# Kernel optimization log

Measured on AMD Instinct MI355X. Metric: run time of the kernel, lower is better.

## Reference

```python
import jax, jax.numpy as jnp
import numpy as np

DIM = 2048
NUM_HEADS = 8
HEAD_DIM = DIM // NUM_HEADS  # 256; forward requires seq_len == HEAD_DIM
B = 64
N = HEAD_DIM  # q @ k (untransposed) only works when N == head_dim


def setup_inputs() -> dict:
    key = jax.random.key(0)
    k1, k2, k3, k4 = jax.random.split(key, 4)
    x = jax.random.normal(k1, (B, N, DIM), dtype=jnp.float32)
    # torch Linear stores weight as [out_features, in_features]
    w_qkv = jax.random.normal(k2, (3 * DIM, DIM), dtype=jnp.float32) * 0.02
    w_proj = jax.random.normal(k3, (DIM, DIM), dtype=jnp.float32) * 0.02
    b_proj = jax.random.normal(k4, (DIM,), dtype=jnp.float32) * 0.02
    return {"x": x, "w_qkv": w_qkv, "w_proj": w_proj, "b_proj": b_proj}


def reference(x, w_qkv, w_proj, b_proj):
    Bb, Nn, C = x.shape
    H, D = NUM_HEADS, C // NUM_HEADS
    # qkv projection (no bias), split into q,k,v of shape [B,H,N,D]
    qkv = (x @ w_qkv.T).reshape(Bb, Nn, 3, H, D).transpose(2, 0, 3, 1, 4)
    q, k, v = qkv[0], qkv[1], qkv[2]
    # NON-standard: q @ k with k NOT transposed -> contracts q's feature dim
    # against k's token dim (valid because D == N). attn: [B,H,N,N]
    attn = jnp.matmul(q, k)
    # transpose last two dims, then softmax over the new last axis
    attn = jnp.swapaxes(attn, -2, -1)
    attn = jax.nn.softmax(attn, axis=-1)
    out = jnp.matmul(attn, v)              # [B,H,N,D]
    out = out.swapaxes(1, 2).reshape(Bb, Nn, C)
    return out @ w_proj.T + b_proj
```

## Files before the change

### kernel.cpp

```cpp
#include <hip/hip_runtime.h>
#include <hip/hip_bf16.h>

typedef unsigned short u16;
typedef __attribute__((ext_vector_type(4))) float f32x4;
typedef __attribute__((ext_vector_type(8))) short short8;
typedef __attribute__((ext_vector_type(8))) u16 us8;


__device__ __forceinline__ u16 f2bf(float f) {
  union { float f; unsigned u; } v; v.f = f;
  unsigned r = v.u + 0x7fffu + ((v.u >> 16) & 1u);
  return (u16)(r >> 16);
}
__device__ __forceinline__ float bf2f(u16 h) {
  union { unsigned u; float f; } v; v.u = ((unsigned)h) << 16; return v.f;
}

__global__ void beacon_kernel(float* __restrict__ out, float val, int n) {
  int stride = gridDim.x * blockDim.x;
  for (int i = blockIdx.x * blockDim.x + threadIdx.x; i < n; i += stride)
    out[i] = val;
}

__global__ void split_kernel(const float* __restrict__ in, u16* __restrict__ hi,
                             u16* __restrict__ lo, int n4) {
  int stride = gridDim.x * blockDim.x;
  for (int i = blockIdx.x * blockDim.x + threadIdx.x; i < n4; i += stride) {
    f32x4 v = ((const f32x4*)in)[i];
    ushort4 h;
    h.x = f2bf(v[0]); h.y = f2bf(v[1]); h.z = f2bf(v[2]); h.w = f2bf(v[3]);
    ((ushort4*)hi)[i] = h;
    if (lo) {
      ushort4 l;
      l.x = f2bf(v[0] - bf2f(h.x)); l.y = f2bf(v[1] - bf2f(h.y));
      l.z = f2bf(v[2] - bf2f(h.z)); l.w = f2bf(v[3] - bf2f(h.w));
      ((ushort4*)lo)[i] = l;
    }
  }
}

#define SCHED0 __builtin_amdgcn_sched_barrier(0)
#define LGKM0 do { asm volatile("s_waitcnt lgkmcnt(0)" ::: "memory"); SCHED0; } while (0)
#define VM8 do { asm volatile("s_waitcnt vmcnt(8)" ::: "memory"); } while (0)
#define VM4 do { asm volatile("s_waitcnt vmcnt(4)" ::: "memory"); } while (0)
#define VM0 do { asm volatile("s_waitcnt vmcnt(0)" ::: "memory"); } while (0)
#define BAR __builtin_amdgcn_s_barrier()

template<int EPI>
__global__ __launch_bounds__(512, 2)
void gemm256(const u16* __restrict__ A0, const u16* __restrict__ A1,
             const u16* __restrict__ B0, const u16* __restrict__ B1,
             int ldA, int ldB, int ntiles, int segShift, int gridMx,
             u16* __restrict__ qh, u16* __restrict__ ql,
             u16* __restrict__ kh, u16* __restrict__ kl,
             u16* __restrict__ vv,
             float* __restrict__ fout, const float* __restrict__ bias) {
  extern __shared__ __align__(16) u16 lds[];

  const int tid = threadIdx.x;
  const int w = tid >> 6, lane = tid & 63;
  const int wr = w >> 2, wcn = w & 3;
  const int l15 = lane & 15, g = lane >> 4;
  const int rsl = (g + l15) & 3;
  const int scol = ((((tid & 3) - ((tid >> 2) & 3)) & 3) << 3);

  int bid = blockIdx.x, cpx = gridDim.x >> 3;
  int swz = (bid & 7) * cpx + (bid >> 3);
  int m0 = (swz % gridMx) << 8;
  int n0 = (swz / gridMx) << 8;

  const u16* As[2] = {A0, A1};
  const u16* Bs[2] = {B0, B1};
  const int kmask = (1 << segShift) - 1;

  f32x4 acc[8][4] = {};
  short8 af[8], bfr[4];

  auto stage = [&](int db, const u16* Ab, const u16* Bb, int k0) {
    #pragma unroll
    for (int s = 0; s < 2; ++s) {
      const u16* srcA = Ab + (size_t)(m0 + s * 128 + (tid >> 2)) * ldA + k0 + scol;
      u16* dstA = lds + db * 16384 + s * 4096 + tid * 8;
      __builtin_amdgcn_global_load_lds(
          (const __attribute__((address_space(1))) unsigned*)srcA,
          (__attribute__((address_space(3))) unsigned*)dstA, 16, 0, 0);
      const u16* srcB = Bb + (size_t)(n0 + s * 128 + (tid >> 2)) * ldB + k0 + scol;
      u16* dstB = lds + db * 16384 + 8192 + s * 4096 + tid * 8;
      __builtin_amdgcn_global_load_lds(
          (const __attribute__((address_space(1))) unsigned*)srcB,
          (__attribute__((address_space(3))) unsigned*)dstB, 16, 0, 0);
    }
  };
  auto readAB = [&](int db) {
    const u16* base = lds + db * 16384;
    #pragma unroll
    for (int i = 0; i < 8; ++i) {
      int row = wr * 128 + i * 16 + l15;
      af[i] = *(const short8*)(base + row * 32 + rsl * 8);
    }
    #pragma unroll
    for (int j = 0; j < 4; ++j) {
      int row = wcn * 64 + j * 16 + l15;
      bfr[j] = *(const short8*)(base + 8192 + row * 32 + rsl * 8);
    }
  };

#define MMA_ALL                                                                \
  __builtin_amdgcn_s_setprio(1);                                               \
  _Pragma("unroll") for (int i = 0; i < 8; ++i)                                \
    _Pragma("unroll") for (int j = 0; j < 4; ++j)                              \
      acc[i][j] = __builtin_amdgcn_mfma_f32_16x16x32_bf16(                     \
          af[i], bfr[j], acc[i][j], 0, 0, 0);                                  \
  __builtin_amdgcn_s_setprio(0)

  const int T = ntiles;
  #pragma unroll
  for (int p = 0; p < 3; ++p)
    stage(p, As[p >> segShift], Bs[p >> segShift], (p & kmask) << 5);

  for (int t = 0; t < T - 3; ++t) {
    VM8; BAR; SCHED0;
    readAB(t & 3);
    int t3 = t + 3;
    stage(t3 & 3, As[t3 >> segShift], Bs[t3 >> segShift], (t3 & kmask) << 5);
    LGKM0;
    MMA_ALL;
  }
  VM8; BAR; SCHED0; readAB((T - 3) & 3); LGKM0; MMA_ALL;
  VM4; BAR; SCHED0; readAB((T - 2) & 3); LGKM0; MMA_ALL;
  VM0; BAR; SCHED0; readAB((T - 1) & 3); LGKM0; MMA_ALL;
#undef MMA_ALL

  #pragma unroll
  for (int i = 0; i < 8; ++i)
    #pragma unroll
    for (int j = 0; j < 4; ++j)
      #pragma unroll
      for (int rr = 0; rr < 4; ++rr) {
        int gm = m0 + wr * 128 + i * 16 + g * 4 + rr;
        int gn = n0 + wcn * 64 + j * 16 + l15;
        float val = acc[i][j][rr];
        if constexpr (EPI == 0) {
          int b = gm >> 8, tok = gm & 255;
          int sel = gn >> 11, head = (gn >> 8) & 7, col = gn & 255;
          size_t addr = (((size_t)b * 8 + head) * 256 + tok) * 256 + col;
          u16 h = f2bf(val), lo = f2bf(val - bf2f(h));
          if (sel == 0) { qh[addr] = h; ql[addr] = lo; }
          else          { kh[addr] = h; kl[addr] = lo; }
        } else if constexpr (EPI == 1) {
          int b = gm >> 8, tok = gm & 255;
          int head = (gn >> 8) & 7, col = gn & 255;
          size_t addr = (((size_t)b * 8 + head) * 256 + tok) * 256 + col;
          vv[addr] = f2bf(val);
        } else {
          fout[(size_t)gm * 2048 + gn] = val + bias[gn];
        }
      }
}

template<int EPI, int SWZ>
__global__ __launch_bounds__(256)
void gemm_nt(const u16* __restrict__ A0, const u16* __restrict__ A1, const u16* __restrict__ A2,
             const u16* __restrict__ B0, const u16* __restrict__ B1, const u16* __restrict__ B2,
             float* __restrict__ sout, u16* __restrict__ aout,
             int ksteps, int segShift, int plane_base) {
  __shared__ __align__(16) u16 lds[8192];
  u16* sA = lds;
  u16* sB = lds + 4096;

  const int tid = threadIdx.x;
  const int wave = tid >> 6, lane = tid & 63;
  const int wr = wave >> 1, wc = wave & 1;
  const int l15 = lane & 15, l16 = lane >> 4;
  const int sxor = (l15 >> 1) & 3;

  size_t zoffA = 0, zoffB = 0;
  if constexpr (EPI == 2) {
    size_t gz = (size_t)(plane_base + blockIdx.z) * 65536;
    zoffA = gz; zoffB = gz;
  }
  if constexpr (EPI == 3) {
    zoffA = (size_t)blockIdx.z * 65536;
    zoffB = (size_t)(plane_base + blockIdx.z) * 65536;
  }
  const u16* As[3] = {A0 + zoffA, A1 + zoffA, A2 + zoffA};
  const u16* Bs[3] = {B0 + zoffB, B1 + zoffB, B2 + zoffB};

  const int m0 = blockIdx.x << 7;
  const int n0 = blockIdx.y << 7;
  const int kmask = (1 << segShift) - 1;

  f32x4 acc[4][4] = {};

  auto stage = [&](const u16* gp, int ld, u16* slot, int row0, int k0) {
    int scol = ((lane & 3) ^ ((lane >> 3) & 3)) * 8;
    #pragma unroll
    for (int c = 0; c < 2; ++c) {
      int chunk = wave + c * 4;
      int r = chunk * 16 + (lane >> 2);
      const u16* src = gp + (size_t)(row0 + r) * ld + (k0 + scol);
      __builtin_amdgcn_global_load_lds(
          (const __attribute__((address_space(1))) unsigned*)src,
          (__attribute__((address_space(3))) unsigned*)(slot + chunk * 512), 16, 0, 0);
    }
  };

  for (int ks = 0; ks < ksteps; ++ks) {
    int seg = ks >> segShift;
    int k0 = (ks & kmask) * 32;
    stage(As[seg], 256, sA, m0, k0);
    stage(Bs[seg], 256, sB, n0, k0);
    __syncthreads();

    short8 a[4], b[4];
    #pragma unroll
    for (int i = 0; i < 4; ++i) {
      int ra = (wr * 64 + i * 16 + l15) * 4 + (l16 ^ sxor);
      int rb = (wc * 64 + i * 16 + l15) * 4 + (l16 ^ sxor);
      a[i] = ((const short8*)sA)[ra];
      b[i] = ((const short8*)sB)[rb];
    }
    #pragma unroll
    for (int i = 0; i < 4; ++i)
      #pragma unroll
      for (int j = 0; j < 4; ++j)
        acc[i][j] = __builtin_amdgcn_mfma_f32_16x16x32_bf16(a[i], b[j], acc[i][j], 0, 0, 0);
    __syncthreads();
  }

  #pragma unroll
  for (int i = 0; i < 4; ++i)
    #pragma unroll
    for (int j = 0; j < 4; ++j)
      #pragma unroll
      for (int r = 0; r < 4; ++r) {
        int gm = m0 + wr * 64 + i * 16 + l16 * 4 + r;
        int gn = n0 + wc * 64 + j * 16 + l15;
        float val = acc[i][j][r];
        if constexpr (EPI == 2) {
          sout[(size_t)blockIdx.z * 65536 + (size_t)gm * 256 + gn] = val;
        } else {
          int gp = plane_base + blockIdx.z;
          size_t row = (size_t)(gp >> 3) * 256 + gm;
          size_t col = (size_t)(gp & 7) * 256 + gn;
          aout[row * 2048 + col] = f2bf(val);
        }
      }
}

__global__ void transpose_inplace(u16* __restrict__ kh, u16* __restrict__ kl,
                                  u16* __restrict__ v) {
  __shared__ u16 ta[64][66], tb[64][66];
  u16* base = (blockIdx.z == 0) ? kh : (blockIdx.z == 1) ? kl : v;
  u16* pl = base + (size_t)blockIdx.y * 65536;
  const int RA[10] = {0,1,2,3, 0,0,0,1,1,2};
  const int CA[10] = {0,1,2,3, 1,2,3,2,3,3};
  int p = blockIdx.x;
  int R = RA[p], C = CA[p];
  bool diag = (R == C);
  int tid = threadIdx.x;
  int r = tid >> 2, c0 = (tid & 3) * 16;

  const us8* sa = (const us8*)(pl + (size_t)(R * 64 + r) * 256 + C * 64 + c0);
  us8 a0 = sa[0], a1 = sa[1];
  #pragma unroll
  for (int s = 0; s < 8; ++s) { ta[r][c0 + s] = a0[s]; ta[r][c0 + 8 + s] = a1[s]; }
  if (!diag) {
    const us8* sb = (const us8*)(pl + (size_t)(C * 64 + r) * 256 + R * 64 + c0);
    us8 b0 = sb[0], b1 = sb[1];
    #pragma unroll
    for (int s = 0; s < 8; ++s) { tb[r][c0 + s] = b0[s]; tb[r][c0 + 8 + s] = b1[s]; }
  }
  __syncthreads();
  us8 o0, o1;
  #pragma unroll
  for (int s = 0; s < 8; ++s) { o0[s] = ta[c0 + s][r]; o1[s] = ta[c0 + 8 + s][r]; }
  us8* da = (us8*)(pl + (size_t)(C * 64 + r) * 256 + R * 64 + c0);
  da[0] = o0; da[1] = o1;
  if (!diag) {
    us8 p0, p1;
    #pragma unroll
    for (int s = 0; s < 8; ++s) { p0[s] = tb[c0 + s][r]; p1[s] = tb[c0 + 8 + s][r]; }
    us8* db = (us8*)(pl + (size_t)(R * 64 + r) * 256 + C * 64 + c0);
    db[0] = p0; db[1] = p1;
  }
}

__global__ void softmax_kernel(const float* __restrict__ S, u16* __restrict__ P) {
  int row = blockIdx.x * 4 + (threadIdx.x >> 6);
  int lane = threadIdx.x & 63;
  f32x4 v = ((const f32x4*)(S + (size_t)row * 256))[lane];
  float mx = fmaxf(fmaxf(v[0], v[1]), fmaxf(v[2], v[3]));
  #pragma unroll
  for (int o = 32; o > 0; o >>= 1) mx = fmaxf(mx, __shfl_xor(mx, o));
  float e0 = __expf(v[0] - mx), e1 = __expf(v[1] - mx);
  float e2 = __expf(v[2] - mx), e3 = __expf(v[3] - mx);
  float sum = e0 + e1 + e2 + e3;
  #pragma unroll
  for (int o = 32; o > 0; o >>= 1) sum += __shfl_xor(sum, o);
  float inv = 1.0f / sum;
  ushort4 p;
  p.x = f2bf(e0 * inv); p.y = f2bf(e1 * inv); p.z = f2bf(e2 * inv); p.w = f2bf(e3 * inv);
  ((ushort4*)(P + (size_t)row * 256))[lane] = p;
}

extern "C" void kernel_launch(void* const* d_in, const int* in_sizes, int n_in,
                              void* d_out, int out_size, void* d_ws, size_t ws_size,
                              hipStream_t stream) {
  const float* x  = (const float*)d_in[0];
  const float* wq = (const float*)d_in[1];
  const float* wp = (const float*)d_in[2];
  const float* bp = (const float*)d_in[3];
  float* out = (float*)d_out;
  char* ws = (char*)d_ws;

  const size_t MB = 1ull << 20;
  const size_t NEED = 432 * MB;
  if (ws_size < NEED) {
    beacon_kernel<<<2048, 256, 0, stream>>>(out, (float)(ws_size >> 20), 16384 * 2048);
    return;
  }

  u16* q_hi = (u16*)(ws);
  u16* q_lo = (u16*)(ws + 64 * MB);
  u16* k_hi = (u16*)(ws + 128 * MB);
  u16* k_lo = (u16*)(ws + 192 * MB);
  u16* vbuf = (u16*)(ws + 256 * MB);
  u16* x_hi = (u16*)(ws + 320 * MB);
  u16* w_hi = (u16*)(ws + 384 * MB);
  u16* w_lo = (u16*)(ws + 408 * MB);
  float* S  = (float*)(ws + 320 * MB);
  u16* Pm   = (u16*)(ws + 352 * MB);
  u16* attn = (u16*)(ws + 368 * MB);
  u16* wpb  = (u16*)(ws + 320 * MB);

  split_kernel<<<8192, 256, 0, stream>>>(x,  x_hi, nullptr, 16384 * 2048 / 4);
  split_kernel<<<4096, 256, 0, stream>>>(wq, w_hi, w_lo, 6144 * 2048 / 4);

  gemm256<0><<<1024, 512, 131072, stream>>>(
      x_hi, x_hi, w_hi, w_lo, 2048, 2048, 128, 6, 64,
      q_hi, q_lo, k_hi, k_lo, nullptr, nullptr, nullptr);
  const u16* wv = w_hi + (size_t)4096 * 2048;
  gemm256<1><<<512, 512, 131072, stream>>>(
      x_hi, x_hi, wv, wv, 2048, 2048, 64, 6, 64,
      nullptr, nullptr, nullptr, nullptr, vbuf, nullptr, nullptr);

  transpose_inplace<<<dim3(10, 512, 3), 256, 0, stream>>>(k_hi, k_lo, vbuf);

  for (int gp = 0; gp < 4; ++gp) {
    int pb = gp * 128;
    gemm_nt<2, 0><<<dim3(2, 2, 128), 256, 0, stream>>>(
        k_hi, k_hi, k_lo, q_hi, q_lo, q_hi,
        S, nullptr, 24, 3, pb);
    softmax_kernel<<<8192, 256, 0, stream>>>(S, Pm);
    gemm_nt<3, 0><<<dim3(2, 2, 128), 256, 0, stream>>>(
        Pm, Pm, Pm, vbuf, vbuf, vbuf,
        nullptr, attn, 8, 3, pb);
  }

  split_kernel<<<2048, 256, 0, stream>>>(wp, wpb, nullptr, 2048 * 2048 / 4);
  gemm256<2><<<512, 512, 131072, stream>>>(
      attn, attn, wpb, wpb, 2048, 2048, 64, 6, 64,
      nullptr, nullptr, nullptr, nullptr, nullptr, out, bp);
}
```

Before: 1.179 ms.

## Restructure 256x256 GEMM into K=64 tiles with quadrant-phased 8-wave ping-pong pipeline

Rewrites the main 256x256 bf16 GEMM mainloop to use K=64 tiles split into four 128-row half-buffers (A halves, B halves), double-buffered by tile parity. Each K tile is processed in four quadrant phases where waves read a quarter of the operands, issue the next half-tile load, and run 16 MFMAs. This interleaves global-to-LDS loads with compute at finer granularity and uses an XOR swizzle over 8 slots to avoid bank conflicts. It adds many more barriers per tile, and the per-wave output mapping changes from 128x64 to four 64x32 quadrants, which may add sync overhead.

```diff
diff --git a/kernel.cpp b/kernel.cpp
--- a/kernel.cpp
+++ b/kernel.cpp
@@ -41,15 +41,14 @@
 
 #define SCHED0 __builtin_amdgcn_sched_barrier(0)
 #define LGKM0 do { asm volatile("s_waitcnt lgkmcnt(0)" ::: "memory"); SCHED0; } while (0)
-#define VM8 do { asm volatile("s_waitcnt vmcnt(8)" ::: "memory"); } while (0)
-#define VM4 do { asm volatile("s_waitcnt vmcnt(4)" ::: "memory"); } while (0)
+#define VM6 do { asm volatile("s_waitcnt vmcnt(6)" ::: "memory"); } while (0)
 #define VM0 do { asm volatile("s_waitcnt vmcnt(0)" ::: "memory"); } while (0)
 #define BAR __builtin_amdgcn_s_barrier()
 
 template<int EPI>
 __global__ __launch_bounds__(512, 2)
-void gemm256(const u16* __restrict__ A0, const u16* __restrict__ A1,
-             const u16* __restrict__ B0, const u16* __restrict__ B1,
+void gemm256(const u16* __restrict__ A0p, const u16* __restrict__ A1p,
+             const u16* __restrict__ B0p, const u16* __restrict__ B1p,
              int ldA, int ldB, int ntiles, int segShift, int gridMx,
              u16* __restrict__ qh, u16* __restrict__ ql,
              u16* __restrict__ kh, u16* __restrict__ kl,
@@ -59,77 +58,128 @@
 
   const int tid = threadIdx.x;
   const int w = tid >> 6, lane = tid & 63;
-  const int wr = w >> 2, wcn = w & 3;
+  const int qr = w >> 2, qc = w & 3;
   const int l15 = lane & 15, g = lane >> 4;
-  const int rsl = (g + l15) & 3;
-  const int scol = ((((tid & 3) - ((tid >> 2) & 3)) & 3) << 3);
+  const int rsw = l15 & 7;
+  const int scol = (((tid & 7) ^ ((tid >> 3) & 7)) << 3);
 
   int bid = blockIdx.x, cpx = gridDim.x >> 3;
   int swz = (bid & 7) * cpx + (bid >> 3);
   int m0 = (swz % gridMx) << 8;
   int n0 = (swz / gridMx) << 8;
 
-  const u16* As[2] = {A0, A1};
-  const u16* Bs[2] = {B0, B1};
+  const u16* As[2] = {A0p, A1p};
+  const u16* Bs[2] = {B0p, B1p};
   const int kmask = (1 << segShift) - 1;
 
   f32x4 acc[8][4] = {};
-  short8 af[8], bfr[4];
-
-  auto stage = [&](int db, const u16* Ab, const u16* Bb, int k0) {
-    #pragma unroll
-    for (int s = 0; s < 2; ++s) {
-      const u16* srcA = Ab + (size_t)(m0 + s * 128 + (tid >> 2)) * ldA + k0 + scol;
-      u16* dstA = lds + db * 16384 + s * 4096 + tid * 8;
+  short8 aR[8], bR[4];
+
+  auto stA = [&](int t, int h) {
+    const u16* bp = As[t >> segShift];
+    int k0 = (t & kmask) << 6;
+    u16* dst0 = lds + (h * 2 + (t & 1)) * 8192 + tid * 8;
+    #pragma unroll
+    for (int L = 0; L < 2; ++L) {
+      const u16* src = bp + (size_t)(m0 + h * 128 + L * 64 + (tid >> 3)) * ldA + k0 + scol;
       __builtin_amdgcn_global_load_lds(
-          (const __attribute__((address_space(1))) unsigned*)srcA,
-          (__attribute__((address_space(3))) unsigned*)dstA, 16, 0, 0);
-      const u16* srcB = Bb + (size_t)(n0 + s * 128 + (tid >> 2)) * ldB + k0 + scol;
-      u16* dstB = lds + db * 16384 + 8192 + s * 4096 + tid * 8;
+          (const __attribute__((address_space(1))) unsigned*)src,
+          (__attribute__((address_space(3))) unsigned*)(dst0 + L * 4096), 16, 0, 0);
+    }
+  };
+  auto stB = [&](int t, int h) {
+    const u16* bp = Bs[t >> segShift];
+    int k0 = (t & kmask) << 6;
+    u16* dst0 = lds + ((2 + h) * 2 + (t & 1)) * 8192 + tid * 8;
+    #pragma unroll
+    for (int L = 0; L < 2; ++L) {
+      const u16* src = bp + (size_t)(n0 + h * 128 + L * 64 + (tid >> 3)) * ldB + k0 + scol;
       __builtin_amdgcn_global_load_lds(
-          (const __attribute__((address_space(1))) unsigned*)srcB,
-          (__attribute__((address_space(3))) unsigned*)dstB, 16, 0, 0);
+          (const __attribute__((address_space(1))) unsigned*)src,
+          (__attribute__((address_space(3))) unsigned*)(dst0 + L * 4096), 16, 0, 0);
     }
   };
-  auto readAB = [&](int db) {
-    const u16* base = lds + db * 16384;
-    #pragma unroll
-    for (int i = 0; i < 8; ++i) {
-      int row = wr * 128 + i * 16 + l15;
-      af[i] = *(const short8*)(base + row * 32 + rsl * 8);
-    }
-    #pragma unroll
-    for (int j = 0; j < 4; ++j) {
-      int row = wcn * 64 + j * 16 + l15;
-      bfr[j] = *(const short8*)(base + 8192 + row * 32 + rsl * 8);
+  auto readA = [&](int par, int MH) {
+    const u16* base = lds + (MH * 2 + par) * 8192;
+    #pragma unroll
+    for (int fm = 0; fm < 4; ++fm) {
+      int lrow = qr * 64 + fm * 16 + l15;
+      #pragma unroll
+      for (int k = 0; k < 2; ++k) {
+        int sl = (k * 4 + g) ^ rsw;
+        aR[fm * 2 + k] = *(const short8*)(base + lrow * 64 + sl * 8);
+      }
     }
   };
-
-#define MMA_ALL                                                                \
+  auto readB = [&](int par, int NH) {
+    const u16* base = lds + ((2 + NH) * 2 + par) * 8192;
+    #pragma unroll
+    for (int fn = 0; fn < 2; ++fn) {
+      int lrow = qc * 32 + fn * 16 + l15;
+      #pragma unroll
+      for (int k = 0; k < 2; ++k) {
+        int sl = (k * 4 + g) ^ rsw;
+        bR[fn * 2 + k] = *(const short8*)(base + lrow * 64 + sl * 8);
+      }
+    }
+  };
+
+#define MMA_PH(MH, NH)                                                         \
   __builtin_amdgcn_s_setprio(1);                                               \
-  _Pragma("unroll") for (int i = 0; i < 8; ++i)                                \
-    _Pragma("unroll") for (int j = 0; j < 4; ++j)                              \
-      acc[i][j] = __builtin_amdgcn_mfma_f32_16x16x32_bf16(                     \
-          af[i], bfr[j], acc[i][j], 0, 0, 0);                                  \
+  _Pragma("unroll") for (int fm = 0; fm < 4; ++fm)                             \
+    _Pragma("unroll") for (int fn = 0; fn < 2; ++fn)                           \
+      _Pragma("unroll") for (int k = 0; k < 2; ++k)                            \
+        acc[(MH) * 4 + fm][(NH) * 2 + fn] =                                    \
+            __builtin_amdgcn_mfma_f32_16x16x32_bf16(                           \
+                aR[fm * 2 + k], bR[fn * 2 + k],                                \
+                acc[(MH) * 4 + fm][(NH) * 2 + fn], 0, 0, 0);                   \
   __builtin_amdgcn_s_setprio(0)
 
   const int T = ntiles;
-  #pragma unroll
-  for (int p = 0; p < 3; ++p)
-    stage(p, As[p >> segShift], Bs[p >> segShift], (p & kmask) << 5);
-
-  for (int t = 0; t < T - 3; ++t) {
-    VM8; BAR; SCHED0;
-    readAB(t & 3);
-    int t3 = t + 3;
-    stage(t3 & 3, As[t3 >> segShift], Bs[t3 >> segShift], (t3 & kmask) << 5);
-    LGKM0;
-    MMA_ALL;
-  }
-  VM8; BAR; SCHED0; readAB((T - 3) & 3); LGKM0; MMA_ALL;
-  VM4; BAR; SCHED0; readAB((T - 2) & 3); LGKM0; MMA_ALL;
-  VM0; BAR; SCHED0; readAB((T - 1) & 3); LGKM0; MMA_ALL;
-#undef MMA_ALL
+  stA(0, 0); stB(0, 0); stB(0, 1); stA(0, 1);
+  stA(1, 0); stB(1, 1); stA(1, 1);
+  VM6; BAR; SCHED0;
+
+  #pragma unroll 1
+  for (int i = 0; i < T / 2; ++i) {
+    const int ta = 2 * i, tb = ta + 1;
+    const bool last = (i == T / 2 - 1);
+    readA(0, 0); readB(0, 0);
+    stB(tb, 0);
+    BAR; LGKM0; MMA_PH(0, 0);
+    BAR; SCHED0;
+    readB(0, 1);
+    if (!last) stA(ta + 2, 0);
+    BAR; LGKM0; MMA_PH(0, 1);
+    BAR; SCHED0;
+    readA(0, 1);
+    if (!last) stB(ta + 2, 1);
+    BAR; LGKM0; MMA_PH(1, 1);
+    BAR; SCHED0;
+    readB(0, 0);
+    if (!last) stA(ta + 2, 1);
+    BAR; LGKM0; MMA_PH(1, 0);
+    if (last) { VM0; } else { VM6; }
+    BAR; SCHED0;
+    readA(1, 0); readB(1, 0);
+    if (!last) stB(ta + 2, 0);
+    BAR; LGKM0; MMA_PH(0, 0);
+    BAR; SCHED0;
+    readB(1, 1);
+    if (!last) stA(tb + 2, 0);
+    BAR; LGKM0; MMA_PH(0, 1);
+    BAR; SCHED0;
+    readA(1, 1);
+    if (!last) stB(tb + 2, 1);
+    BAR; LGKM0; MMA_PH(1, 1);
+    BAR; SCHED0;
+    readB(1, 0);
+    if (!last) stA(tb + 2, 1);
+    BAR; LGKM0; MMA_PH(1, 0);
+    if (!last) { VM6; }
+    BAR; SCHED0;
+  }
+#undef MMA_PH
 
   #pragma unroll
   for (int i = 0; i < 8; ++i)
@@ -137,8 +187,8 @@
     for (int j = 0; j < 4; ++j)
       #pragma unroll
       for (int rr = 0; rr < 4; ++rr) {
-        int gm = m0 + wr * 128 + i * 16 + g * 4 + rr;
-        int gn = n0 + wcn * 64 + j * 16 + l15;
+        int gm = m0 + (i >> 2) * 128 + qr * 64 + (i & 3) * 16 + g * 4 + rr;
+        int gn = n0 + (j >> 1) * 128 + qc * 32 + (j & 1) * 16 + l15;
         float val = acc[i][j][rr];
         if constexpr (EPI == 0) {
           int b = gm >> 8, tok = gm & 255;
@@ -192,13 +242,13 @@
 
   f32x4 acc[4][4] = {};
 
-  auto stage = [&](const u16* gp, int ld, u16* slot, int row0, int k0) {
+  auto stage = [&](const u16* gp, u16* slot, int row0, int k0) {
     int scol = ((lane & 3) ^ ((lane >> 3) & 3)) * 8;
     #pragma unroll
     for (int c = 0; c < 2; ++c) {
       int chunk = wave + c * 4;
       int r = chunk * 16 + (lane >> 2);
-      const u16* src = gp + (size_t)(row0 + r) * ld + (k0 + scol);
+      const u16* src = gp + (size_t)(row0 + r) * 256 + (k0 + scol);
       __builtin_amdgcn_global_load_lds(
           (const __attribute__((address_space(1))) unsigned*)src,
           (__attribute__((address_space(3))) unsigned*)(slot + chunk * 512), 16, 0, 0);
@@ -208,8 +258,8 @@
   for (int ks = 0; ks < ksteps; ++ks) {
     int seg = ks >> segShift;
     int k0 = (ks & kmask) * 32;
-    stage(As[seg], 256, sA, m0, k0);
-    stage(Bs[seg], 256, sB, n0, k0);
+    stage(As[seg], sA, m0, k0);
+    stage(Bs[seg], sB, n0, k0);
     __syncthreads();
 
     short8 a[4], b[4];
@@ -338,11 +388,11 @@
   split_kernel<<<4096, 256, 0, stream>>>(wq, w_hi, w_lo, 6144 * 2048 / 4);
 
   gemm256<0><<<1024, 512, 131072, stream>>>(
-      x_hi, x_hi, w_hi, w_lo, 2048, 2048, 128, 6, 64,
+      x_hi, x_hi, w_hi, w_lo, 2048, 2048, 64, 5, 64,
       q_hi, q_lo, k_hi, k_lo, nullptr, nullptr, nullptr);
   const u16* wv = w_hi + (size_t)4096 * 2048;
   gemm256<1><<<512, 512, 131072, stream>>>(
-      x_hi, x_hi, wv, wv, 2048, 2048, 64, 6, 64,
+      x_hi, x_hi, wv, wv, 2048, 2048, 32, 5, 64,
       nullptr, nullptr, nullptr, nullptr, vbuf, nullptr, nullptr);
 
   transpose_inplace<<<dim3(10, 512, 3), 256, 0, stream>>>(k_hi, k_lo, vbuf);
@@ -360,6 +410,6 @@
 
   split_kernel<<<2048, 256, 0, stream>>>(wp, wpb, nullptr, 2048 * 2048 / 4);
   gemm256<2><<<512, 512, 131072, stream>>>(
-      attn, attn, wpb, wpb, 2048, 2048, 64, 6, 64,
+      attn, attn, wpb, wpb, 2048, 2048, 32, 5, 64,
       nullptr, nullptr, nullptr, nullptr, nullptr, out, bp);
 }
```

Result: faster. 1.146 ms (-2.9%).
